# Kernel optimization log

Measured on AMD Instinct MI355X. Metric: run time of the kernel, lower is better.

## Reference

```python
import jax, jax.numpy as jnp
import numpy as np

H = 56; W = 56; WS = 7; SHIFT = 3; HEADS = 4; C = 128; B = 64
N = WS * WS            # 49 tokens per window
NW = (H // WS) * (W // WS)  # 64 windows per image
HD = C // HEADS
EPS = 1e-5


def _rel_index():
    # matches get_relative_index: pairwise coord diffs in [-(WS-1), WS-1];
    # torch negative indexing wraps, so take mod (2*WS-1)
    coords = np.array([[i, j] for i in range(WS) for j in range(WS)])
    rel = coords[None, :, :] - coords[:, None, :]          # (N, N, 2)
    return (rel % (2 * WS - 1)).astype(np.int32)


def _attn_mask():
    # matches get_attn_mask for shifted windows
    img = np.zeros((H, W))
    sl = (slice(0, -WS), slice(-WS, -SHIFT), slice(-SHIFT, None))
    cnt = 0
    for hs in sl:
        for ws_ in sl:
            img[hs, ws_] = cnt
            cnt += 1
    m = img.reshape(H // WS, WS, W // WS, WS).transpose(0, 2, 1, 3).reshape(NW, N)
    am = m[:, None, :] - m[:, :, None]                     # (NW, N, N)
    return np.where(am != 0, -100.0, 0.0).astype(np.float32)

_REL_IDX = _rel_index()
_MASK = _attn_mask()


def _layernorm(x, g, b):
    mu = jnp.mean(x, axis=-1, keepdims=True)
    var = jnp.mean(jnp.square(x - mu), axis=-1, keepdims=True)
    return (x - mu) * jax.lax.rsqrt(var + EPS) * g + b


def setup_inputs() -> dict:
    key = jax.random.key(0)
    ks = jax.random.split(key, 16)
    s = 0.02
    return {
        "x": jax.random.normal(ks[0], (B, H * W, C), jnp.float32),
        "wq": jax.random.normal(ks[1], (C, C), jnp.float32) * s,
        "bq": jnp.zeros((C,), jnp.float32),
        "wk": jax.random.normal(ks[2], (C, C), jnp.float32) * s,
        "bk": jnp.zeros((C,), jnp.float32),
        "wv": jax.random.normal(ks[3], (C, C), jnp.float32) * s,
        "bv": jnp.zeros((C,), jnp.float32),
        "wo": jax.random.normal(ks[4], (C, C), jnp.float32) * s,
        "bo": jnp.zeros((C,), jnp.float32),
        "rel_table": jax.random.normal(ks[5], (2 * WS - 1, 2 * WS - 1, HEADS), jnp.float32) * s,
        "ln1_g": jnp.ones((C,), jnp.float32),
        "ln1_b": jnp.zeros((C,), jnp.float32),
        "ln2_g": jnp.ones((C,), jnp.float32),
        "ln2_b": jnp.zeros((C,), jnp.float32),
        "w1": jax.random.normal(ks[6], (C, 4 * C), jnp.float32) * s,
        "b1": jnp.zeros((4 * C,), jnp.float32),
        "w2": jax.random.normal(ks[7], (4 * C, C), jnp.float32) * s,
        "b2": jnp.zeros((C,), jnp.float32),
    }


def reference(x, wq, bq, wk, bk, wv, bv, wo, bo, rel_table,
              ln1_g, ln1_b, ln2_g, ln2_b, w1, b1, w2, b2):
    shortcut = x                                     # (B, H*W, C)
    h = _layernorm(x, ln1_g, ln1_b).reshape(B, H, W, C)
    h = jnp.roll(h, (-SHIFT, -SHIFT), axis=(1, 2))   # cyclic shift
    # window partition -> (B*NW, N, C)
    h = h.reshape(B, H // WS, WS, W // WS, WS, C).transpose(0, 1, 3, 2, 4, 5)
    h = h.reshape(B * NW, N, C)
    q = (h @ wq + bq).reshape(B * NW, N, HEADS, HD)
    k = (h @ wk + bk).reshape(B * NW, N, HEADS, HD)
    v = (h @ wv + bv).reshape(B * NW, N, HEADS, HD)
    attn = jnp.einsum('nqhd,nkhd->nhqk', q, k) / np.sqrt(HD).astype(np.float32)
    bias = rel_table[_REL_IDX[:, :, 0], _REL_IDX[:, :, 1]]  # (N, N, HEADS)
    attn = attn + jnp.transpose(bias, (2, 0, 1))[None]      # (1, H, N, N)
    # shifted-window additive mask
    attn = attn.reshape(B, NW, HEADS, N, N) + jnp.asarray(_MASK)[None, :, None]
    attn = jax.nn.softmax(attn.reshape(B * NW, HEADS, N, N), axis=-1)
    out = jnp.einsum('nhqk,nkhd->nqhd', attn, v).reshape(B * NW, N, C)
    out = out @ wo + bo
    # faithful to source bug: output taken directly from window-ordered tokens
    h = out.reshape(B, H * W, C)
    h = h + shortcut
    m = _layernorm(h, ln2_g, ln2_b)
    m = jax.nn.gelu(m @ w1 + b1, approximate=False) @ w2 + b2
    return h + m
```

## Files before the change

kernel.cpp:

```cpp
#include <hip/hip_runtime.h>

typedef __attribute__((ext_vector_type(8))) short short8;
typedef __attribute__((ext_vector_type(4))) float f32x4;
typedef unsigned short u16;
typedef unsigned int u32;

#define MFMA16(a, b, c) __builtin_amdgcn_mfma_f32_16x16x32_bf16((a), (b), (c), 0, 0, 0)
#define SCALE_Q 0.1767766952966369f

__device__ __forceinline__ u16 f2bf(float x) {
  u32 u = __float_as_uint(x);
  u32 r = u + 0x7FFF + ((u >> 16) & 1);
  return (u16)(r >> 16);
}

__device__ __forceinline__ float gelu_f(float x) {
  float u = 0.7978845608f * (x + 0.044715f * x * x * x);
  float e = __expf(2.f * u);
  float t = 1.f - 2.f / (e + 1.f);
  return 0.5f * x * (1.f + t);
}

__global__ __launch_bounds__(256) void k0_weights(
    const float* __restrict__ wq, const float* __restrict__ wk, const float* __restrict__ wv,
    const float* __restrict__ wo, const float* __restrict__ w1, const float* __restrict__ w2,
    const float* __restrict__ bq, const float* __restrict__ bk, const float* __restrict__ bv,
    u16* __restrict__ wqkvt, u16* __restrict__ wot, u16* __restrict__ w1t, u16* __restrict__ w2t,
    float* __restrict__ bqkv) {
  int idx = blockIdx.x * 256 + threadIdx.x;
  if (idx < 49152) {
    int n = idx >> 7, k = idx & 127;
    float v;
    if (n < 128) v = wq[k * 128 + n] * SCALE_Q;
    else if (n < 256) v = wk[k * 128 + (n - 128)];
    else v = wv[k * 128 + (n - 256)];
    wqkvt[idx] = f2bf(v);
  } else if (idx < 65536) {
    int j = idx - 49152;
    int n = j >> 7, k = j & 127;
    wot[j] = f2bf(wo[k * 128 + n]);
  } else if (idx < 131072) {
    int j = idx - 65536;
    int n = j >> 7, k = j & 127;
    w1t[j] = f2bf(w1[k * 512 + n]);
  } else if (idx < 196608) {
    int j = idx - 131072;
    int n = j >> 9, k = j & 511;
    w2t[j] = f2bf(w2[k * 128 + n]);
  } else if (idx < 196992) {
    int n = idx - 196608;
    float v;
    if (n < 128) v = bq[n] * SCALE_Q;
    else if (n < 256) v = bk[n - 128];
    else v = bv[n - 256];
    bqkv[n] = v;
  }
}

__global__ __launch_bounds__(256) void k0_biasmask(const float* __restrict__ rel, float* __restrict__ bm) {
  int idx = blockIdx.x * 256 + threadIdx.x;
  int reg = idx & 3;
  int lane = (idx >> 2) & 63;
  int nt = (idx >> 8) & 3;
  int mt = (idx >> 10) & 3;
  int h = (idx >> 12) & 3;
  int wi = idx >> 14;
  int r = mt * 16 + ((lane >> 4) << 2) + reg;
  int c = nt * 16 + (lane & 15);
  float v = -1e30f;
  if (r < 49 && c < 49) {
    int qr = r / 7, qc = r % 7, kr = c / 7, kc = c % 7;
    int i0 = (kr - qr + 13) % 13, i1 = (kc - qc + 13) % 13;
    v = rel[(i0 * 13 + i1) * 4 + h];
    int gh = (wi >> 3) * 7 + qr, gw = (wi & 7) * 7 + qc;
    int kh = (wi >> 3) * 7 + kr, kw = (wi & 7) * 7 + kc;
    int rq = (gh < 49 ? 0 : (gh < 53 ? 1 : 2)) * 3 + (gw < 49 ? 0 : (gw < 53 ? 1 : 2));
    int rk = (kh < 49 ? 0 : (kh < 53 ? 1 : 2)) * 3 + (kw < 49 ? 0 : (kw < 53 ? 1 : 2));
    if (rq != rk) v -= 100.f;
  }
  bm[idx] = v;
}

__global__ __launch_bounds__(256) void k1_ln1(const float* __restrict__ x, const float* __restrict__ g,
                                              const float* __restrict__ b, u16* __restrict__ hwin) {
  int wid = threadIdx.x >> 6, lane = threadIdx.x & 63;
  int t = blockIdx.x * 4 + wid;
  float2 v = *(const float2*)(x + t * 128 + lane * 2);
  float s = v.x + v.y;
#pragma unroll
  for (int o = 1; o < 64; o <<= 1) s += __shfl_xor(s, o);
  float mu = s * 0.0078125f;
  float dx = v.x - mu, dy = v.y - mu;
  float q = dx * dx + dy * dy;
#pragma unroll
  for (int o = 1; o < 64; o <<= 1) q += __shfl_xor(q, o);
  float rstd = rsqrtf(q * 0.0078125f + 1e-5f);
  float y0 = dx * rstd * g[lane * 2] + b[lane * 2];
  float y1 = dy * rstd * g[lane * 2 + 1] + b[lane * 2 + 1];
  int bi = t / 3136, hw = t - bi * 3136;
  int oh = hw / 56, ow = hw - oh * 56;
  int gh = oh - 3; if (gh < 0) gh += 56;
  int gw = ow - 3; if (gw < 0) gw += 56;
  int win = bi * 64 + (gh / 7) * 8 + gw / 7;
  int n = (gh % 7) * 7 + (gw % 7);
  u32 packed = (u32)f2bf(y0) | ((u32)f2bf(y1) << 16);
  *(u32*)(hwin + (win * 49 + n) * 128 + lane * 2) = packed;
}

__global__ __launch_bounds__(256) void k2_qkv(const u16* __restrict__ hwin, const u16* __restrict__ wt,
                                              const float* __restrict__ bqkv, u16* __restrict__ qb,
                                              u16* __restrict__ kb, u16* __restrict__ vt) {
  int tid = threadIdx.x, lane = tid & 63, w = tid >> 6;
  int g = lane >> 4, l15 = lane & 15;
  int row0 = blockIdx.x * 256 + w * 64;
  short8 a[4][4];
#pragma unroll
  for (int mt = 0; mt < 4; ++mt)
#pragma unroll
    for (int kt = 0; kt < 4; ++kt)
      a[mt][kt] = *(const short8*)(hwin + (size_t)(row0 + mt * 16 + l15) * 128 + kt * 32 + g * 8);
  const f32x4 vz = {0.f, 0.f, 0.f, 0.f};
  for (int nb = 0; nb < 6; ++nb) {
    f32x4 acc[4][4];
#pragma unroll
    for (int i = 0; i < 4; ++i)
#pragma unroll
      for (int j = 0; j < 4; ++j) acc[i][j] = vz;
#pragma unroll
    for (int kt = 0; kt < 4; ++kt) {
      short8 bfr[4];
#pragma unroll
      for (int nt = 0; nt < 4; ++nt)
        bfr[nt] = *(const short8*)(wt + (size_t)(nb * 64 + nt * 16 + l15) * 128 + kt * 32 + g * 8);
#pragma unroll
      for (int mt = 0; mt < 4; ++mt)
#pragma unroll
        for (int nt = 0; nt < 4; ++nt) acc[mt][nt] = MFMA16(a[mt][kt], bfr[nt], acc[mt][nt]);
    }
#pragma unroll
    for (int mt = 0; mt < 4; ++mt)
#pragma unroll
      for (int nt = 0; nt < 4; ++nt) {
        int ng = nb * 64 + nt * 16 + l15;
        float bias = bqkv[ng];
#pragma unroll
        for (int reg = 0; reg < 4; ++reg) {
          int token = row0 + mt * 16 + g * 4 + reg;
          u16 hv = f2bf(acc[mt][nt][reg] + bias);
          if (nb < 2) qb[(size_t)token * 128 + ng] = hv;
          else if (nb < 4) kb[(size_t)token * 128 + ng - 128] = hv;
          else {
            int c = ng - 256;
            int win = token / 49, nn = token - win * 49;
            vt[(size_t)win * 8192 + c * 64 + nn] = hv;
          }
        }
      }
  }
}

__global__ __launch_bounds__(256) void k3_attn(const u16* __restrict__ qb, const u16* __restrict__ kb,
                                               const u16* __restrict__ vt, const float* __restrict__ bm,
                                               u16* __restrict__ ao) {
  __shared__ u16 pl[4 * 4096];
  int win = blockIdx.x;
  int lane = threadIdx.x & 63, head = threadIdx.x >> 6;
  int g = lane >> 4, l15 = lane & 15;
  u16* myp = pl + head * 4096;
  short8 aq[4], bk_[4];
#pragma unroll
  for (int mt = 0; mt < 4; ++mt)
    aq[mt] = *(const short8*)(qb + (size_t)(win * 49 + mt * 16 + l15) * 128 + head * 32 + g * 8);
#pragma unroll
  for (int nt = 0; nt < 4; ++nt)
    bk_[nt] = *(const short8*)(kb + (size_t)(win * 49 + nt * 16 + l15) * 128 + head * 32 + g * 8);
  const f32x4* bmv = (const f32x4*)bm + ((win & 63) * 4 + head) * 1024;
  f32x4 s[4][4];
#pragma unroll
  for (int mt = 0; mt < 4; ++mt)
#pragma unroll
    for (int nt = 0; nt < 4; ++nt) s[mt][nt] = bmv[(mt * 4 + nt) * 64 + lane];
#pragma unroll
  for (int mt = 0; mt < 4; ++mt)
#pragma unroll
    for (int nt = 0; nt < 4; ++nt) s[mt][nt] = MFMA16(aq[mt], bk_[nt], s[mt][nt]);
#pragma unroll
  for (int mt = 0; mt < 4; ++mt)
#pragma unroll
    for (int reg = 0; reg < 4; ++reg) {
      float m = fmaxf(fmaxf(s[mt][0][reg], s[mt][1][reg]), fmaxf(s[mt][2][reg], s[mt][3][reg]));
#pragma unroll
      for (int o = 1; o < 16; o <<= 1) m = fmaxf(m, __shfl_xor(m, o));
      float p0 = __expf(s[mt][0][reg] - m);
      float p1 = __expf(s[mt][1][reg] - m);
      float p2 = __expf(s[mt][2][reg] - m);
      float p3 = __expf(s[mt][3][reg] - m);
      float sum = p0 + p1 + p2 + p3;
#pragma unroll
      for (int o = 1; o < 16; o <<= 1) sum += __shfl_xor(sum, o);
      float rinv = 1.f / sum;
      s[mt][0][reg] = p0 * rinv; s[mt][1][reg] = p1 * rinv;
      s[mt][2][reg] = p2 * rinv; s[mt][3][reg] = p3 * rinv;
    }
#pragma unroll
  for (int mt = 0; mt < 4; ++mt)
#pragma unroll
    for (int nt = 0; nt < 4; ++nt)
#pragma unroll
      for (int reg = 0; reg < 4; ++reg) {
        int r = mt * 16 + g * 4 + reg, c = nt * 16 + l15;
        int byte_ = ((r << 7) + (c << 1)) ^ ((r & 7) << 4);
        *(u16*)((char*)myp + byte_) = f2bf(s[mt][nt][reg]);
      }
  __syncthreads();
  short8 vb[2][2];
#pragma unroll
  for (int kk = 0; kk < 2; ++kk)
#pragma unroll
    for (int n2 = 0; n2 < 2; ++n2)
      vb[kk][n2] = *(const short8*)(vt + (size_t)win * 8192 + (head * 32 + n2 * 16 + l15) * 64 + kk * 32 + g * 8);
  const f32x4 vz = {0.f, 0.f, 0.f, 0.f};
  f32x4 o[4][2];
#pragma unroll
  for (int mt = 0; mt < 4; ++mt) { o[mt][0] = vz; o[mt][1] = vz; }
#pragma unroll
  for (int mt = 0; mt < 4; ++mt)
#pragma unroll
    for (int kk = 0; kk < 2; ++kk) {
      int r = mt * 16 + l15;
      int byte_ = ((r << 7) + kk * 64 + g * 16) ^ ((r & 7) << 4);
      short8 pa = *(const short8*)((const char*)myp + byte_);
#pragma unroll
      for (int n2 = 0; n2 < 2; ++n2) o[mt][n2] = MFMA16(pa, vb[kk][n2], o[mt][n2]);
    }
#pragma unroll
  for (int mt = 0; mt < 4; ++mt)
#pragma unroll
    for (int n2 = 0; n2 < 2; ++n2)
#pragma unroll
      for (int reg = 0; reg < 4; ++reg) {
        int r = mt * 16 + g * 4 + reg;
        if (r < 49) ao[(size_t)(win * 49 + r) * 128 + head * 32 + n2 * 16 + l15] = f2bf(o[mt][n2][reg]);
      }
}

__global__ __launch_bounds__(256) void k4_proj(const u16* __restrict__ ao, const u16* __restrict__ wot,
                                               const float* __restrict__ bo, const float* __restrict__ x,
                                               const float* __restrict__ g2, const float* __restrict__ b2,
                                               float* __restrict__ dout, u16* __restrict__ ln2) {
  int tid = threadIdx.x, lane = tid & 63, w = tid >> 6;
  int g = lane >> 4, l15 = lane & 15;
  int row0 = blockIdx.x * 256 + w * 64;
  short8 a[4][4];
#pragma unroll
  for (int mt = 0; mt < 4; ++mt)
#pragma unroll
    for (int kt = 0; kt < 4; ++kt)
      a[mt][kt] = *(const short8*)(ao + (size_t)(row0 + mt * 16 + l15) * 128 + kt * 32 + g * 8);
  const f32x4 vz = {0.f, 0.f, 0.f, 0.f};
  f32x4 acc[4][8];
#pragma unroll
  for (int i = 0; i < 4; ++i)
#pragma unroll
    for (int j = 0; j < 8; ++j) acc[i][j] = vz;
#pragma unroll
  for (int kt = 0; kt < 4; ++kt) {
    short8 bfr[8];
#pragma unroll
    for (int nt = 0; nt < 8; ++nt)
      bfr[nt] = *(const short8*)(wot + (size_t)(nt * 16 + l15) * 128 + kt * 32 + g * 8);
#pragma unroll
    for (int mt = 0; mt < 4; ++mt)
#pragma unroll
      for (int nt = 0; nt < 8; ++nt) acc[mt][nt] = MFMA16(a[mt][kt], bfr[nt], acc[mt][nt]);
  }
#pragma unroll
  for (int mt = 0; mt < 4; ++mt)
#pragma unroll
    for (int reg = 0; reg < 4; ++reg) {
      int token = row0 + mt * 16 + g * 4 + reg;
      float hv[8];
      float s1 = 0.f, s2 = 0.f;
#pragma unroll
      for (int nt = 0; nt < 8; ++nt) {
        int c = nt * 16 + l15;
        float v = acc[mt][nt][reg] + bo[c] + x[(size_t)token * 128 + c];
        dout[(size_t)token * 128 + c] = v;
        hv[nt] = v; s1 += v; s2 += v * v;
      }
#pragma unroll
      for (int o = 1; o < 16; o <<= 1) { s1 += __shfl_xor(s1, o); s2 += __shfl_xor(s2, o); }
      float mu = s1 * 0.0078125f;
      float rstd = rsqrtf(fmaxf(s2 * 0.0078125f - mu * mu, 0.f) + 1e-5f);
#pragma unroll
      for (int nt = 0; nt < 8; ++nt) {
        int c = nt * 16 + l15;
        ln2[(size_t)token * 128 + c] = f2bf((hv[nt] - mu) * rstd * g2[c] + b2[c]);
      }
    }
}

__global__ __launch_bounds__(256) void k5_mlp1(const u16* __restrict__ ln2, const u16* __restrict__ w1t,
                                               const float* __restrict__ b1, u16* __restrict__ g1) {
  int tid = threadIdx.x, lane = tid & 63, w = tid >> 6;
  int g = lane >> 4, l15 = lane & 15;
  int row0 = blockIdx.x * 256 + w * 64;
  short8 a[4][4];
#pragma unroll
  for (int mt = 0; mt < 4; ++mt)
#pragma unroll
    for (int kt = 0; kt < 4; ++kt)
      a[mt][kt] = *(const short8*)(ln2 + (size_t)(row0 + mt * 16 + l15) * 128 + kt * 32 + g * 8);
  const f32x4 vz = {0.f, 0.f, 0.f, 0.f};
  for (int nb = 0; nb < 8; ++nb) {
    f32x4 acc[4][4];
#pragma unroll
    for (int i = 0; i < 4; ++i)
#pragma unroll
      for (int j = 0; j < 4; ++j) acc[i][j] = vz;
#pragma unroll
    for (int kt = 0; kt < 4; ++kt) {
      short8 bfr[4];
#pragma unroll
      for (int nt = 0; nt < 4; ++nt)
        bfr[nt] = *(const short8*)(w1t + (size_t)(nb * 64 + nt * 16 + l15) * 128 + kt * 32 + g * 8);
#pragma unroll
      for (int mt = 0; mt < 4; ++mt)
#pragma unroll
        for (int nt = 0; nt < 4; ++nt) acc[mt][nt] = MFMA16(a[mt][kt], bfr[nt], acc[mt][nt]);
    }
#pragma unroll
    for (int mt = 0; mt < 4; ++mt)
#pragma unroll
      for (int nt = 0; nt < 4; ++nt) {
        int ng = nb * 64 + nt * 16 + l15;
        float bias = b1[ng];
#pragma unroll
        for (int reg = 0; reg < 4; ++reg) {
          int token = row0 + mt * 16 + g * 4 + reg;
          g1[(size_t)token * 512 + ng] = f2bf(gelu_f(acc[mt][nt][reg] + bias));
        }
      }
  }
}

__global__ __launch_bounds__(256) void k6_mlp2(const u16* __restrict__ g1, const u16* __restrict__ w2t,
                                               const float* __restrict__ b2, float* __restrict__ dout) {
  int tid = threadIdx.x, lane = tid & 63, w = tid >> 6;
  int g = lane >> 4, l15 = lane & 15;
  int row0 = blockIdx.x * 256 + w * 64;
  const f32x4 vz = {0.f, 0.f, 0.f, 0.f};
  f32x4 acc[4][8];
#pragma unroll
  for (int i = 0; i < 4; ++i)
#pragma unroll
    for (int j = 0; j < 8; ++j) acc[i][j] = vz;
#pragma unroll
  for (int kt = 0; kt < 16; ++kt) {
    short8 a[4];
#pragma unroll
    for (int mt = 0; mt < 4; ++mt)
      a[mt] = *(const short8*)(g1 + (size_t)(row0 + mt * 16 + l15) * 512 + kt * 32 + g * 8);
    short8 bfr[8];
#pragma unroll
    for (int nt = 0; nt < 8; ++nt)
      bfr[nt] = *(const short8*)(w2t + (size_t)(nt * 16 + l15) * 512 + kt * 32 + g * 8);
#pragma unroll
    for (int mt = 0; mt < 4; ++mt)
#pragma unroll
      for (int nt = 0; nt < 8; ++nt) acc[mt][nt] = MFMA16(a[mt], bfr[nt], acc[mt][nt]);
  }
#pragma unroll
  for (int mt = 0; mt < 4; ++mt)
#pragma unroll
    for (int nt = 0; nt < 8; ++nt) {
      int c = nt * 16 + l15;
      float bias = b2[c];
#pragma unroll
      for (int reg = 0; reg < 4; ++reg) {
        int token = row0 + mt * 16 + g * 4 + reg;
        size_t i = (size_t)token * 128 + c;
        dout[i] = acc[mt][nt][reg] + bias + dout[i];
      }
    }
}

extern "C" void kernel_launch(void* const* d_in, const int* in_sizes, int n_in,
                              void* d_out, int out_size, void* d_ws, size_t ws_size,
                              hipStream_t stream) {
  const float* x    = (const float*)d_in[0];
  const float* wq   = (const float*)d_in[1];
  const float* bq   = (const float*)d_in[2];
  const float* wk   = (const float*)d_in[3];
  const float* bk   = (const float*)d_in[4];
  const float* wv   = (const float*)d_in[5];
  const float* bv   = (const float*)d_in[6];
  const float* wo   = (const float*)d_in[7];
  const float* bo   = (const float*)d_in[8];
  const float* rel  = (const float*)d_in[9];
  const float* ln1g = (const float*)d_in[10];
  const float* ln1b = (const float*)d_in[11];
  const float* ln2g = (const float*)d_in[12];
  const float* ln2b = (const float*)d_in[13];
  const float* w1   = (const float*)d_in[14];
  const float* b1   = (const float*)d_in[15];
  const float* w2   = (const float*)d_in[16];
  const float* b2   = (const float*)d_in[17];
  float* out = (float*)d_out;
  char* ws = (char*)d_ws;

  const size_t TOK = 200704;
  float* bmask = (float*)(ws);
  u16* wqkvt = (u16*)(ws + (size_t)(4 << 20));
  u16* wot   = (u16*)(ws + (size_t)(4 << 20) + 196608);
  u16* w1t   = (u16*)(ws + (size_t)(4 << 20) + 229376);
  u16* w2t   = (u16*)(ws + (size_t)(4 << 20) + 360448);
  float* bqkv = (float*)(ws + (size_t)(4 << 20) + 491520);
  const size_t SB = TOK * 128 * 2;
  u16* hwin = (u16*)(ws + (size_t)(8 << 20));
  u16* qb   = (u16*)(ws + (size_t)(8 << 20) + SB);
  u16* kb   = (u16*)(ws + (size_t)(8 << 20) + 2 * SB);
  u16* vt   = (u16*)(ws + (size_t)(8 << 20) + 3 * SB);
  u16* attn = hwin;
  u16* ln2  = qb;
  u16* g1b  = kb;

  k0_weights<<<770, 256, 0, stream>>>(wq, wk, wv, wo, w1, w2, bq, bk, bv,
                                      wqkvt, wot, w1t, w2t, bqkv);
  k0_biasmask<<<4096, 256, 0, stream>>>(rel, bmask);
  k1_ln1<<<50176, 256, 0, stream>>>(x, ln1g, ln1b, hwin);
  k2_qkv<<<784, 256, 0, stream>>>(hwin, wqkvt, bqkv, qb, kb, vt);
  k3_attn<<<4096, 256, 0, stream>>>(qb, kb, vt, bmask, attn);
  k4_proj<<<784, 256, 0, stream>>>(attn, wot, bo, x, ln2g, ln2b, out, ln2);
  k5_mlp1<<<784, 256, 0, stream>>>(ln2, w1t, b1, g1b);
  k6_mlp2<<<784, 256, 0, stream>>>(g1b, w2t, b2, out);
}
```

Before: 892.3 us.

## Fuse output projection into attention and fuse MLP layers via shared memory

Attention now also does the output projection, residual add and LN2 per window. The attention output is staged in shared memory instead of a global buffer. The two MLP GEMMs are merged into one kernel that keeps the GELU hidden activations in LDS, which removes the 512-wide intermediate round trip through HBM. Q/K/V stores become paired 32-bit writes in row layout, with V transposed inside LDS in the attention kernel rather than by scattered global writes. The QKV tile is halved to double the grid. The cost is lower MFMA reuse per block and more LDS use and syncs.

```diff
diff --git a/kernel.cpp b/kernel.cpp
--- a/kernel.cpp
+++ b/kernel.cpp
@@ -7,6 +7,7 @@
 
 #define MFMA16(a, b, c) __builtin_amdgcn_mfma_f32_16x16x32_bf16((a), (b), (c), 0, 0, 0)
 #define SCALE_Q 0.1767766952966369f
+#define TOKENS 200704
 
 __device__ __forceinline__ u16 f2bf(float x) {
   u32 u = __float_as_uint(x);
@@ -19,6 +20,11 @@
   float e = __expf(2.f * u);
   float t = 1.f - 2.f / (e + 1.f);
   return 0.5f * x * (1.f + t);
+}
+
+__device__ __forceinline__ u32 pairpack(u16 me, int lane) {
+  u32 pv = (u32)__shfl_xor((int)me, 1);
+  return (u32)me | (pv << 16);
 }
 
 __global__ __launch_bounds__(256) void k0_weights(
@@ -85,7 +91,7 @@
                                               const float* __restrict__ b, u16* __restrict__ hwin) {
   int wid = threadIdx.x >> 6, lane = threadIdx.x & 63;
   int t = blockIdx.x * 4 + wid;
-  float2 v = *(const float2*)(x + t * 128 + lane * 2);
+  float2 v = *(const float2*)(x + (size_t)t * 128 + lane * 2);
   float s = v.x + v.y;
 #pragma unroll
   for (int o = 1; o < 64; o <<= 1) s += __shfl_xor(s, o);
@@ -104,26 +110,26 @@
   int win = bi * 64 + (gh / 7) * 8 + gw / 7;
   int n = (gh % 7) * 7 + (gw % 7);
   u32 packed = (u32)f2bf(y0) | ((u32)f2bf(y1) << 16);
-  *(u32*)(hwin + (win * 49 + n) * 128 + lane * 2) = packed;
+  *(u32*)(hwin + (size_t)(win * 49 + n) * 128 + lane * 2) = packed;
 }
 
 __global__ __launch_bounds__(256) void k2_qkv(const u16* __restrict__ hwin, const u16* __restrict__ wt,
                                               const float* __restrict__ bqkv, u16* __restrict__ qb,
-                                              u16* __restrict__ kb, u16* __restrict__ vt) {
+                                              u16* __restrict__ kb, u16* __restrict__ vb) {
   int tid = threadIdx.x, lane = tid & 63, w = tid >> 6;
   int g = lane >> 4, l15 = lane & 15;
-  int row0 = blockIdx.x * 256 + w * 64;
-  short8 a[4][4];
-#pragma unroll
-  for (int mt = 0; mt < 4; ++mt)
+  int row0 = blockIdx.x * 128 + w * 32;
+  short8 a[2][4];
+#pragma unroll
+  for (int mt = 0; mt < 2; ++mt)
 #pragma unroll
     for (int kt = 0; kt < 4; ++kt)
       a[mt][kt] = *(const short8*)(hwin + (size_t)(row0 + mt * 16 + l15) * 128 + kt * 32 + g * 8);
   const f32x4 vz = {0.f, 0.f, 0.f, 0.f};
   for (int nb = 0; nb < 6; ++nb) {
-    f32x4 acc[4][4];
-#pragma unroll
-    for (int i = 0; i < 4; ++i)
+    f32x4 acc[2][4];
+#pragma unroll
+    for (int i = 0; i < 2; ++i)
 #pragma unroll
       for (int j = 0; j < 4; ++j) acc[i][j] = vz;
 #pragma unroll
@@ -133,39 +139,66 @@
       for (int nt = 0; nt < 4; ++nt)
         bfr[nt] = *(const short8*)(wt + (size_t)(nb * 64 + nt * 16 + l15) * 128 + kt * 32 + g * 8);
 #pragma unroll
-      for (int mt = 0; mt < 4; ++mt)
+      for (int mt = 0; mt < 2; ++mt)
 #pragma unroll
         for (int nt = 0; nt < 4; ++nt) acc[mt][nt] = MFMA16(a[mt][kt], bfr[nt], acc[mt][nt]);
     }
-#pragma unroll
-    for (int mt = 0; mt < 4; ++mt)
+    u16* dst; int cb;
+    if (nb < 2) { dst = qb; cb = nb * 64; }
+    else if (nb < 4) { dst = kb; cb = (nb - 2) * 64; }
+    else { dst = vb; cb = (nb - 4) * 64; }
+#pragma unroll
+    for (int mt = 0; mt < 2; ++mt)
 #pragma unroll
       for (int nt = 0; nt < 4; ++nt) {
-        int ng = nb * 64 + nt * 16 + l15;
-        float bias = bqkv[ng];
+        int c = cb + nt * 16 + l15;
+        float bias = bqkv[nb * 64 + nt * 16 + l15];
 #pragma unroll
         for (int reg = 0; reg < 4; ++reg) {
           int token = row0 + mt * 16 + g * 4 + reg;
-          u16 hv = f2bf(acc[mt][nt][reg] + bias);
-          if (nb < 2) qb[(size_t)token * 128 + ng] = hv;
-          else if (nb < 4) kb[(size_t)token * 128 + ng - 128] = hv;
-          else {
-            int c = ng - 256;
-            int win = token / 49, nn = token - win * 49;
-            vt[(size_t)win * 8192 + c * 64 + nn] = hv;
-          }
+          u16 me = f2bf(acc[mt][nt][reg] + bias);
+          u32 word = pairpack(me, lane);
+          if (!(lane & 1)) *(u32*)(dst + (size_t)token * 128 + c) = word;
         }
       }
   }
 }
 
 __global__ __launch_bounds__(256) void k3_attn(const u16* __restrict__ qb, const u16* __restrict__ kb,
-                                               const u16* __restrict__ vt, const float* __restrict__ bm,
-                                               u16* __restrict__ ao) {
-  __shared__ u16 pl[4 * 4096];
+                                               const u16* __restrict__ vb, const float* __restrict__ bm,
+                                               const u16* __restrict__ wot, const float* __restrict__ bo,
+                                               const float* __restrict__ x, const float* __restrict__ g2,
+                                               const float* __restrict__ b2, float* __restrict__ dout,
+                                               u16* __restrict__ ln2) {
+  __shared__ u16 smem[16384 + 8192];
+  u16* pl = smem;
+  u16* vtl = smem + 16384;
+  u16* aol = smem;
   int win = blockIdx.x;
-  int lane = threadIdx.x & 63, head = threadIdx.x >> 6;
+  int tid = threadIdx.x;
+  int lane = tid & 63, head = tid >> 6;
   int g = lane >> 4, l15 = lane & 15;
+
+  {
+    int t = tid >> 2, dq = tid & 3;
+    long grow = (long)win * 49 + t;
+    bool valid = (t < 49) && (grow < TOKENS);
+    short8 r[4];
+#pragma unroll
+    for (int c = 0; c < 4; ++c) {
+      if (valid) r[c] = *(const short8*)(vb + grow * 128 + dq * 32 + c * 8);
+      else r[c] = short8{0, 0, 0, 0, 0, 0, 0, 0};
+    }
+#pragma unroll
+    for (int c = 0; c < 4; ++c)
+#pragma unroll
+      for (int e = 0; e < 8; ++e) {
+        int d = dq * 32 + c * 8 + e;
+        int byte_ = (d * 128 + t * 2) ^ ((((d & 7) ^ ((d >> 3) & 7))) << 4);
+        *(u16*)((char*)vtl + byte_) = (u16)r[c][e];
+      }
+  }
+
   u16* myp = pl + head * 4096;
   short8 aq[4], bk_[4];
 #pragma unroll
@@ -213,12 +246,16 @@
         *(u16*)((char*)myp + byte_) = f2bf(s[mt][nt][reg]);
       }
   __syncthreads();
-  short8 vb[2][2];
+
+  short8 vf[2][2];
 #pragma unroll
   for (int kk = 0; kk < 2; ++kk)
 #pragma unroll
-    for (int n2 = 0; n2 < 2; ++n2)
-      vb[kk][n2] = *(const short8*)(vt + (size_t)win * 8192 + (head * 32 + n2 * 16 + l15) * 64 + kk * 32 + g * 8);
+    for (int n2 = 0; n2 < 2; ++n2) {
+      int d = head * 32 + n2 * 16 + l15;
+      int byte_ = (d * 128 + (kk * 32 + g * 8) * 2) ^ ((((d & 7) ^ ((d >> 3) & 7))) << 4);
+      vf[kk][n2] = *(const short8*)((const char*)vtl + byte_);
+    }
   const f32x4 vz = {0.f, 0.f, 0.f, 0.f};
   f32x4 o[4][2];
 #pragma unroll
@@ -231,61 +268,53 @@
       int byte_ = ((r << 7) + kk * 64 + g * 16) ^ ((r & 7) << 4);
       short8 pa = *(const short8*)((const char*)myp + byte_);
 #pragma unroll
-      for (int n2 = 0; n2 < 2; ++n2) o[mt][n2] = MFMA16(pa, vb[kk][n2], o[mt][n2]);
-    }
+      for (int n2 = 0; n2 < 2; ++n2) o[mt][n2] = MFMA16(pa, vf[kk][n2], o[mt][n2]);
+    }
+  __syncthreads();
+
 #pragma unroll
   for (int mt = 0; mt < 4; ++mt)
 #pragma unroll
     for (int n2 = 0; n2 < 2; ++n2)
 #pragma unroll
       for (int reg = 0; reg < 4; ++reg) {
-        int r = mt * 16 + g * 4 + reg;
-        if (r < 49) ao[(size_t)(win * 49 + r) * 128 + head * 32 + n2 * 16 + l15] = f2bf(o[mt][n2][reg]);
-      }
-}
-
-__global__ __launch_bounds__(256) void k4_proj(const u16* __restrict__ ao, const u16* __restrict__ wot,
-                                               const float* __restrict__ bo, const float* __restrict__ x,
-                                               const float* __restrict__ g2, const float* __restrict__ b2,
-                                               float* __restrict__ dout, u16* __restrict__ ln2) {
-  int tid = threadIdx.x, lane = tid & 63, w = tid >> 6;
-  int g = lane >> 4, l15 = lane & 15;
-  int row0 = blockIdx.x * 256 + w * 64;
-  short8 a[4][4];
-#pragma unroll
-  for (int mt = 0; mt < 4; ++mt)
-#pragma unroll
-    for (int kt = 0; kt < 4; ++kt)
-      a[mt][kt] = *(const short8*)(ao + (size_t)(row0 + mt * 16 + l15) * 128 + kt * 32 + g * 8);
-  const f32x4 vz = {0.f, 0.f, 0.f, 0.f};
-  f32x4 acc[4][8];
-#pragma unroll
-  for (int i = 0; i < 4; ++i)
-#pragma unroll
-    for (int j = 0; j < 8; ++j) acc[i][j] = vz;
+        int r = mt * 16 + g * 4 + reg, c = head * 32 + n2 * 16 + l15;
+        u16 me = f2bf(o[mt][n2][reg]);
+        u32 word = pairpack(me, lane);
+        if (!(lane & 1)) {
+          int byte_ = ((r << 8) + c * 2) ^ ((r & 7) << 4);
+          *(u32*)((char*)aol + byte_) = word;
+        }
+      }
+  __syncthreads();
+
+  int w = head;
+  f32x4 pacc[8];
+#pragma unroll
+  for (int nt = 0; nt < 8; ++nt) pacc[nt] = vz;
 #pragma unroll
   for (int kt = 0; kt < 4; ++kt) {
-    short8 bfr[8];
-#pragma unroll
-    for (int nt = 0; nt < 8; ++nt)
-      bfr[nt] = *(const short8*)(wot + (size_t)(nt * 16 + l15) * 128 + kt * 32 + g * 8);
-#pragma unroll
-    for (int mt = 0; mt < 4; ++mt)
-#pragma unroll
-      for (int nt = 0; nt < 8; ++nt) acc[mt][nt] = MFMA16(a[mt][kt], bfr[nt], acc[mt][nt]);
-  }
-#pragma unroll
-  for (int mt = 0; mt < 4; ++mt)
-#pragma unroll
-    for (int reg = 0; reg < 4; ++reg) {
-      int token = row0 + mt * 16 + g * 4 + reg;
+    int row = w * 16 + l15;
+    int byte_ = ((row << 8) + kt * 64 + g * 16) ^ ((row & 7) << 4);
+    short8 af = *(const short8*)((const char*)aol + byte_);
+#pragma unroll
+    for (int nt = 0; nt < 8; ++nt) {
+      short8 bf = *(const short8*)(wot + (size_t)(nt * 16 + l15) * 128 + kt * 32 + g * 8);
+      pacc[nt] = MFMA16(af, bf, pacc[nt]);
+    }
+  }
+#pragma unroll
+  for (int reg = 0; reg < 4; ++reg) {
+    int row = w * 16 + g * 4 + reg;
+    if (row < 49) {
+      size_t token = (size_t)win * 49 + row;
       float hv[8];
       float s1 = 0.f, s2 = 0.f;
 #pragma unroll
       for (int nt = 0; nt < 8; ++nt) {
         int c = nt * 16 + l15;
-        float v = acc[mt][nt][reg] + bo[c] + x[(size_t)token * 128 + c];
-        dout[(size_t)token * 128 + c] = v;
+        float v = pacc[nt][reg] + bo[c] + x[token * 128 + c];
+        dout[token * 128 + c] = v;
         hv[nt] = v; s1 += v; s2 += v * v;
       }
 #pragma unroll
@@ -295,94 +324,95 @@
 #pragma unroll
       for (int nt = 0; nt < 8; ++nt) {
         int c = nt * 16 + l15;
-        ln2[(size_t)token * 128 + c] = f2bf((hv[nt] - mu) * rstd * g2[c] + b2[c]);
-      }
-    }
-}
-
-__global__ __launch_bounds__(256) void k5_mlp1(const u16* __restrict__ ln2, const u16* __restrict__ w1t,
-                                               const float* __restrict__ b1, u16* __restrict__ g1) {
+        u16 me = f2bf((hv[nt] - mu) * rstd * g2[c] + b2[c]);
+        u32 word = pairpack(me, lane);
+        if (!(lane & 1)) *(u32*)(ln2 + token * 128 + c) = word;
+      }
+    }
+  }
+}
+
+__global__ __launch_bounds__(256) void k5_mlp(const u16* __restrict__ ln2, const u16* __restrict__ w1t,
+                                              const float* __restrict__ b1, const u16* __restrict__ w2t,
+                                              const float* __restrict__ b2, float* __restrict__ dout) {
+  __shared__ u16 h1[64 * 512];
   int tid = threadIdx.x, lane = tid & 63, w = tid >> 6;
   int g = lane >> 4, l15 = lane & 15;
-  int row0 = blockIdx.x * 256 + w * 64;
-  short8 a[4][4];
-#pragma unroll
-  for (int mt = 0; mt < 4; ++mt)
+  int row0 = blockIdx.x * 64;
+  const f32x4 vz = {0.f, 0.f, 0.f, 0.f};
+
+  {
+    int r0 = w * 16;
+    short8 a[4];
 #pragma unroll
     for (int kt = 0; kt < 4; ++kt)
-      a[mt][kt] = *(const short8*)(ln2 + (size_t)(row0 + mt * 16 + l15) * 128 + kt * 32 + g * 8);
-  const f32x4 vz = {0.f, 0.f, 0.f, 0.f};
-  for (int nb = 0; nb < 8; ++nb) {
-    f32x4 acc[4][4];
-#pragma unroll
-    for (int i = 0; i < 4; ++i)
-#pragma unroll
-      for (int j = 0; j < 4; ++j) acc[i][j] = vz;
-#pragma unroll
-    for (int kt = 0; kt < 4; ++kt) {
-      short8 bfr[4];
-#pragma unroll
-      for (int nt = 0; nt < 4; ++nt)
-        bfr[nt] = *(const short8*)(w1t + (size_t)(nb * 64 + nt * 16 + l15) * 128 + kt * 32 + g * 8);
-#pragma unroll
-      for (int mt = 0; mt < 4; ++mt)
-#pragma unroll
-        for (int nt = 0; nt < 4; ++nt) acc[mt][nt] = MFMA16(a[mt][kt], bfr[nt], acc[mt][nt]);
+      a[kt] = *(const short8*)(ln2 + (size_t)(row0 + r0 + l15) * 128 + kt * 32 + g * 8);
+    for (int nb = 0; nb < 8; ++nb) {
+      f32x4 acc[4];
+#pragma unroll
+      for (int j = 0; j < 4; ++j) acc[j] = vz;
+#pragma unroll
+      for (int kt = 0; kt < 4; ++kt) {
+        short8 bf[4];
+#pragma unroll
+        for (int nt = 0; nt < 4; ++nt)
+          bf[nt] = *(const short8*)(w1t + (size_t)(nb * 64 + nt * 16 + l15) * 128 + kt * 32 + g * 8);
+#pragma unroll
+        for (int nt = 0; nt < 4; ++nt) acc[nt] = MFMA16(a[kt], bf[nt], acc[nt]);
+      }
+#pragma unroll
+      for (int nt = 0; nt < 4; ++nt) {
+        float bias = b1[nb * 64 + nt * 16 + l15];
+#pragma unroll
+        for (int reg = 0; reg < 4; ++reg) {
+          int r = r0 + g * 4 + reg;
+          int c = nb * 64 + nt * 16 + l15;
+          u16 me = f2bf(gelu_f(acc[nt][reg] + bias));
+          u32 word = pairpack(me, lane);
+          if (!(lane & 1)) {
+            int byte_ = (r * 1024 + c * 2) ^ ((r & 7) << 4);
+            *(u32*)((char*)h1 + byte_) = word;
+          }
+        }
+      }
+    }
+  }
+  __syncthreads();
+
+  {
+    int c0 = w * 32;
+    f32x4 acc2[4][2];
+#pragma unroll
+    for (int i = 0; i < 4; ++i) { acc2[i][0] = vz; acc2[i][1] = vz; }
+#pragma unroll
+    for (int kt = 0; kt < 16; ++kt) {
+      short8 bf[2];
+#pragma unroll
+      for (int n2 = 0; n2 < 2; ++n2)
+        bf[n2] = *(const short8*)(w2t + (size_t)(c0 + n2 * 16 + l15) * 512 + kt * 32 + g * 8);
+#pragma unroll
+      for (int mt = 0; mt < 4; ++mt) {
+        int r = mt * 16 + l15;
+        int byte_ = (r * 1024 + kt * 64 + g * 16) ^ ((r & 7) << 4);
+        short8 af = *(const short8*)((const char*)h1 + byte_);
+#pragma unroll
+        for (int n2 = 0; n2 < 2; ++n2) acc2[mt][n2] = MFMA16(af, bf[n2], acc2[mt][n2]);
+      }
     }
 #pragma unroll
     for (int mt = 0; mt < 4; ++mt)
 #pragma unroll
-      for (int nt = 0; nt < 4; ++nt) {
-        int ng = nb * 64 + nt * 16 + l15;
-        float bias = b1[ng];
+      for (int n2 = 0; n2 < 2; ++n2) {
+        int c = c0 + n2 * 16 + l15;
+        float bias = b2[c];
 #pragma unroll
         for (int reg = 0; reg < 4; ++reg) {
-          int token = row0 + mt * 16 + g * 4 + reg;
-          g1[(size_t)token * 512 + ng] = f2bf(gelu_f(acc[mt][nt][reg] + bias));
+          size_t token = (size_t)row0 + mt * 16 + g * 4 + reg;
+          size_t i = token * 128 + c;
+          dout[i] = acc2[mt][n2][reg] + bias + dout[i];
         }
       }
   }
-}
-
-__global__ __launch_bounds__(256) void k6_mlp2(const u16* __restrict__ g1, const u16* __restrict__ w2t,
-                                               const float* __restrict__ b2, float* __restrict__ dout) {
-  int tid = threadIdx.x, lane = tid & 63, w = tid >> 6;
-  int g = lane >> 4, l15 = lane & 15;
-  int row0 = blockIdx.x * 256 + w * 64;
-  const f32x4 vz = {0.f, 0.f, 0.f, 0.f};
-  f32x4 acc[4][8];
-#pragma unroll
-  for (int i = 0; i < 4; ++i)
-#pragma unroll
-    for (int j = 0; j < 8; ++j) acc[i][j] = vz;
-#pragma unroll
-  for (int kt = 0; kt < 16; ++kt) {
-    short8 a[4];
-#pragma unroll
-    for (int mt = 0; mt < 4; ++mt)
-      a[mt] = *(const short8*)(g1 + (size_t)(row0 + mt * 16 + l15) * 512 + kt * 32 + g * 8);
-    short8 bfr[8];
-#pragma unroll
-    for (int nt = 0; nt < 8; ++nt)
-      bfr[nt] = *(const short8*)(w2t + (size_t)(nt * 16 + l15) * 512 + kt * 32 + g * 8);
-#pragma unroll
-    for (int mt = 0; mt < 4; ++mt)
-#pragma unroll
-      for (int nt = 0; nt < 8; ++nt) acc[mt][nt] = MFMA16(a[mt], bfr[nt], acc[mt][nt]);
-  }
-#pragma unroll
-  for (int mt = 0; mt < 4; ++mt)
-#pragma unroll
-    for (int nt = 0; nt < 8; ++nt) {
-      int c = nt * 16 + l15;
-      float bias = b2[c];
-#pragma unroll
-      for (int reg = 0; reg < 4; ++reg) {
-        int token = row0 + mt * 16 + g * 4 + reg;
-        size_t i = (size_t)token * 128 + c;
-        dout[i] = acc[mt][nt][reg] + bias + dout[i];
-      }
-    }
 }
 
 extern "C" void kernel_launch(void* const* d_in, const int* in_sizes, int n_in,
@@ -409,29 +439,24 @@
   float* out = (float*)d_out;
   char* ws = (char*)d_ws;
 
-  const size_t TOK = 200704;
   float* bmask = (float*)(ws);
   u16* wqkvt = (u16*)(ws + (size_t)(4 << 20));
   u16* wot   = (u16*)(ws + (size_t)(4 << 20) + 196608);
   u16* w1t   = (u16*)(ws + (size_t)(4 << 20) + 229376);
   u16* w2t   = (u16*)(ws + (size_t)(4 << 20) + 360448);
   float* bqkv = (float*)(ws + (size_t)(4 << 20) + 491520);
-  const size_t SB = TOK * 128 * 2;
+  const size_t SB = (size_t)TOKENS * 128 * 2;
   u16* hwin = (u16*)(ws + (size_t)(8 << 20));
   u16* qb   = (u16*)(ws + (size_t)(8 << 20) + SB);
   u16* kb   = (u16*)(ws + (size_t)(8 << 20) + 2 * SB);
-  u16* vt   = (u16*)(ws + (size_t)(8 << 20) + 3 * SB);
-  u16* attn = hwin;
-  u16* ln2  = qb;
-  u16* g1b  = kb;
+  u16* vb   = (u16*)(ws + (size_t)(8 << 20) + 3 * SB);
+  u16* ln2  = hwin;
 
   k0_weights<<<770, 256, 0, stream>>>(wq, wk, wv, wo, w1, w2, bq, bk, bv,
                                       wqkvt, wot, w1t, w2t, bqkv);
   k0_biasmask<<<4096, 256, 0, stream>>>(rel, bmask);
   k1_ln1<<<50176, 256, 0, stream>>>(x, ln1g, ln1b, hwin);
-  k2_qkv<<<784, 256, 0, stream>>>(hwin, wqkvt, bqkv, qb, kb, vt);
-  k3_attn<<<4096, 256, 0, stream>>>(qb, kb, vt, bmask, attn);
-  k4_proj<<<784, 256, 0, stream>>>(attn, wot, bo, x, ln2g, ln2b, out, ln2);
-  k5_mlp1<<<784, 256, 0, stream>>>(ln2, w1t, b1, g1b);
-  k6_mlp2<<<784, 256, 0, stream>>>(g1b, w2t, b2, out);
-}
+  k2_qkv<<<1568, 256, 0, stream>>>(hwin, wqkvt, bqkv, qb, kb, vb);
+  k3_attn<<<4096, 256, 0, stream>>>(qb, kb, vb, bmask, wot, bo, x, ln2g, ln2b, out, ln2);
+  k5_mlp<<<3136, 256, 0, stream>>>(ln2, w1t, b1, w2t, b2, out);
+}
```

Result: no change. 884.3 us (-0.9%).
